# Kernel optimization log

Measured on AMD Instinct MI355X. Metric: run time of the kernel, lower is better.

Reference implementation:

```python
import jax, jax.numpy as jnp
import numpy as np

B, S, D = 2, 2048, 1024
H, L = 16, 64  # num_heads, latent_dim (head dim); head_dim = H*L = 1024
ROPE_BASE = 10000.0


def _rope_tables(seq_len, dim):
    inv_freq = 1.0 / (ROPE_BASE ** (2.0 * jnp.arange(0, dim // 2, dtype=jnp.float32) / dim))
    pos = jnp.arange(seq_len, dtype=jnp.float32)
    ang = pos[:, None] * inv_freq[None, :]           # [S, L/2]
    cos = jnp.cos(ang).reshape(1, seq_len, 1, dim // 2)
    sin = jnp.sin(ang).reshape(1, seq_len, 1, dim // 2)
    return cos, sin


def _apply_rope(t, cos, sin):
    # t: [B, S, H, L]; interleaved-pair rotation then concat halves (as in source)
    tr = t.reshape(*t.shape[:-1], -1, 2)             # [B,S,H,L/2,2]
    x0, x1 = tr[..., 0], tr[..., 1]
    out = jnp.concatenate([x0 * cos - x1 * sin, x0 * sin + x1 * cos], axis=-1)
    return out.reshape(t.shape)


def setup_inputs() -> dict:
    key = jax.random.key(0)
    ks = jax.random.split(key, 5)
    scale = 0.03  # ~xavier for 1024x1024
    return {
        "x": jax.random.normal(ks[0], (B, S, D), dtype=jnp.float32),
        "Wq": jax.random.normal(ks[1], (D, H * L), dtype=jnp.float32) * scale,
        "bq": jnp.zeros((H * L,), dtype=jnp.float32),
        "Wk": jax.random.normal(ks[2], (D, H * L), dtype=jnp.float32) * scale,
        "bk": jnp.zeros((H * L,), dtype=jnp.float32),
        "Wv": jax.random.normal(ks[3], (D, H * L), dtype=jnp.float32) * scale,
        "bv": jnp.zeros((H * L,), dtype=jnp.float32),
        "Wo": jax.random.normal(ks[4], (H * L, D), dtype=jnp.float32) * scale,
        "bo": jnp.zeros((D,), dtype=jnp.float32),
    }


def reference(x, Wq, bq, Wk, bk, Wv, bv, Wo, bo):
    b, s, _ = x.shape
    q = (x @ Wq + bq).reshape(b, s, H, L)
    k = (x @ Wk + bk).reshape(b, s, H, L)
    v = (x @ Wv + bv).reshape(b, s, H, L)
    cos, sin = _rope_tables(s, L)
    q = _apply_rope(q, cos, sin)
    k = _apply_rope(k, cos, sin)
    q = jnp.transpose(q, (0, 2, 1, 3))  # [B,H,S,L]
    k = jnp.transpose(k, (0, 2, 1, 3))
    v = jnp.transpose(v, (0, 2, 1, 3))
    scores = jnp.einsum('bnqd,bnkd->bnqk', q, k) / jnp.sqrt(jnp.float32(L))
    # causal mask: keep positions where key <= query
    causal = jnp.arange(s)[None, :] <= jnp.arange(s)[:, None]  # [S,S]
    scores = jnp.where(causal, scores, -1e9)
    attn = jax.nn.softmax(scores, axis=-1)
    attended = jnp.einsum('bnqk,bnkd->bnqd', attn, v)
    attended = jnp.transpose(attended, (0, 2, 1, 3)).reshape(b, s, H * L)
    return attended @ Wo + bo
```

## Files before the change

### kernel.cpp

```cpp
#include <hip/hip_runtime.h>
#include <hip/hip_bf16.h>

typedef __bf16 bf16_t;
typedef __bf16 bf16x2 __attribute__((ext_vector_type(2)));
typedef __bf16 bf16x4 __attribute__((ext_vector_type(4)));
typedef __bf16 bf16x8 __attribute__((ext_vector_type(8)));
typedef float  f32x4  __attribute__((ext_vector_type(4)));

#define GLDS16(gp, lp) __builtin_amdgcn_global_load_lds( \
    (const __attribute__((address_space(1))) void*)(gp), \
    (__attribute__((address_space(3))) void*)(lp), 16, 0, 0)

#define MFMA16(a, b, c) __builtin_amdgcn_mfma_f32_16x16x32_bf16((a), (b), (c), 0, 0, 0)

static constexpr int kB = 2, kS = 2048, kD = 1024, kH = 16, kL = 64;
static constexpr int kM = kB * kS;
static constexpr int kNqkv = 3 * kD;
static constexpr int kBH = kB * kH;

__global__ void cast_x_kernel(const float* __restrict__ x, bf16_t* __restrict__ xb) {
    int i = blockIdx.x * 256 + threadIdx.x;
    float4 v = ((const float4*)x)[i];
    bf16x4 o;
    o[0] = (bf16_t)v.x; o[1] = (bf16_t)v.y; o[2] = (bf16_t)v.z; o[3] = (bf16_t)v.w;
    ((bf16x4*)xb)[i] = o;
}

__global__ void wtrans_kernel(const float* __restrict__ Wq, const float* __restrict__ Wk,
                              const float* __restrict__ Wv, const float* __restrict__ Wo,
                              bf16_t* __restrict__ Wqkv, bf16_t* __restrict__ WoT) {
    __shared__ float t[32 * 33];
    const int z = blockIdx.z;
    const float* W = (z == 0) ? Wq : (z == 1) ? Wk : (z == 2) ? Wv : Wo;
    bf16_t* Wt = (z < 3) ? (Wqkv + (size_t)z * 1024 * 1024) : WoT;
    const int k0 = blockIdx.x * 32, n0 = blockIdx.y * 32;
    const int tid = threadIdx.x;
#pragma unroll
    for (int i = 0; i < 4; ++i) {
        int idx = i * 256 + tid;
        int r = idx >> 5, c = idx & 31;
        t[r * 33 + c] = W[(size_t)(k0 + r) * 1024 + n0 + c];
    }
    __syncthreads();
#pragma unroll
    for (int i = 0; i < 4; ++i) {
        int idx = i * 256 + tid;
        int r = idx >> 5, c = idx & 31;
        Wt[(size_t)(n0 + r) * 1024 + k0 + c] = (bf16_t)t[c * 33 + r];
    }
}

__global__ void rope_table_kernel(float* __restrict__ cosT, float* __restrict__ sinT) {
    int i = blockIdx.x * 256 + threadIdx.x;
    int s = i >> 5, j = i & 31;
    double inv = pow(10000.0, -2.0 * (double)j / 64.0);
    double ang = (double)s * inv;
    cosT[i] = (float)cos(ang);
    sinT[i] = (float)sin(ang);
}

template <int MODE>
__global__ __launch_bounds__(256, 2)
void gemm_bf16(const bf16_t* __restrict__ A, const bf16_t* __restrict__ Bt,
               void* __restrict__ Cout,
               const float* __restrict__ b0, const float* __restrict__ b1,
               const float* __restrict__ b2, int Ndim, int Kdim) {
    __shared__ __align__(16) bf16_t Alds[128 * 32];
    __shared__ __align__(16) bf16_t Blds[128 * 32];
    const int tid = threadIdx.x;
    const int lane = tid & 63;
    const int wid = tid >> 6;
    const int lo = lane & 15, hi = lane >> 4;
    const int bm = blockIdx.x, bn = blockIdx.y;
    const int wr = wid >> 1, wc = wid & 1;

    const int rowS = (wid * 2) * 16 + (lane >> 2);
    const int colE = (lane & 3) * 8;
    const bf16_t* gA0 = A + (size_t)(bm * 128 + rowS) * Kdim + colE;
    const bf16_t* gA1 = gA0 + (size_t)16 * Kdim;
    const bf16_t* gB0 = Bt + (size_t)(bn * 128 + rowS) * Kdim + colE;
    const bf16_t* gB1 = gB0 + (size_t)16 * Kdim;
    bf16_t* lA0 = &Alds[(wid * 2) * 512];
    bf16_t* lA1 = &Alds[(wid * 2 + 1) * 512];
    bf16_t* lB0 = &Blds[(wid * 2) * 512];
    bf16_t* lB1 = &Blds[(wid * 2 + 1) * 512];

    f32x4 acc[4][4];
#pragma unroll
    for (int m = 0; m < 4; ++m)
#pragma unroll
        for (int n = 0; n < 4; ++n) acc[m][n] = (f32x4){0.f, 0.f, 0.f, 0.f};

    const int nk = Kdim >> 5;
    for (int kt = 0; kt < nk; ++kt) {
        const int k0 = kt * 32;
        GLDS16(gA0 + k0, lA0);
        GLDS16(gA1 + k0, lA1);
        GLDS16(gB0 + k0, lB0);
        GLDS16(gB1 + k0, lB1);
        __syncthreads();
        bf16x8 aF[4], bF[4];
#pragma unroll
        for (int m = 0; m < 4; ++m)
            aF[m] = *(const bf16x8*)&Alds[(wr * 64 + m * 16 + lo) * 32 + hi * 8];
#pragma unroll
        for (int n = 0; n < 4; ++n)
            bF[n] = *(const bf16x8*)&Blds[(wc * 64 + n * 16 + lo) * 32 + hi * 8];
#pragma unroll
        for (int m = 0; m < 4; ++m)
#pragma unroll
            for (int n = 0; n < 4; ++n)
                acc[m][n] = MFMA16(aF[m], bF[n], acc[m][n]);
        __syncthreads();
    }

    const int rbase = bm * 128 + wr * 64 + hi * 4;
    const int cbase = bn * 128 + wc * 64 + lo;
    if (MODE == 0) {
        bf16_t* C = (bf16_t*)Cout;
#pragma unroll
        for (int m = 0; m < 4; ++m)
#pragma unroll
            for (int n = 0; n < 4; ++n) {
                const int col = cbase + n * 16;
                const float bias = (col < 1024) ? b0[col]
                                 : (col < 2048) ? b1[col - 1024] : b2[col - 2048];
#pragma unroll
                for (int r = 0; r < 4; ++r) {
                    const int row = rbase + m * 16 + r;
                    C[(size_t)row * Ndim + col] = (bf16_t)(acc[m][n][r] + bias);
                }
            }
    } else {
        float* C = (float*)Cout;
#pragma unroll
        for (int m = 0; m < 4; ++m)
#pragma unroll
            for (int n = 0; n < 4; ++n) {
                const int col = cbase + n * 16;
                const float bias = b0[col];
#pragma unroll
                for (int r = 0; r < 4; ++r) {
                    const int row = rbase + m * 16 + r;
                    C[(size_t)row * Ndim + col] = acc[m][n][r] + bias;
                }
            }
    }
}

__global__ __launch_bounds__(256)
void rope_qk_kernel(const bf16_t* __restrict__ qkv,
                    const float* __restrict__ cosT,
                    const float* __restrict__ sinT,
                    bf16_t* __restrict__ Qr, bf16_t* __restrict__ Kr) {
    const int st = blockIdx.x, bh = blockIdx.y;
    const int b = bh >> 4, h = bh & 15;
    const int tid = threadIdx.x;
    const int r = tid >> 2;
    const int part = tid & 3;
    const int s = st * 64 + r;
    const int bs = b * kS + s;
    const bf16_t* qp = qkv + (size_t)bs * kNqkv + h * 64 + part * 16;
    const bf16_t* kp = qp + 1024;
    const size_t outoff = ((size_t)(b * kH + h) * kS + s) * 64;
    bf16_t* qo = Qr + outoff;
    char*   kob = (char*)(Kr + outoff);
    const float* cr = cosT + s * 32 + part * 8;
    const float* sr = sinT + s * 32 + part * 8;
    const float kScale = 0.125f * 1.44269504f;

    bf16x8 q0 = *(const bf16x8*)qp;
    bf16x8 q1 = *(const bf16x8*)(qp + 8);
    bf16x8 k0 = *(const bf16x8*)kp;
    bf16x8 k1 = *(const bf16x8*)(kp + 8);
    bf16x8 qlo, qhi, klo, khi;
#pragma unroll
    for (int j = 0; j < 8; ++j) {
        const float cv = cr[j];
        const float sv = sr[j];
        float qa, qb2, ka, kb2;
        if (j < 4) {
            qa = (float)q0[2 * j];     qb2 = (float)q0[2 * j + 1];
            ka = (float)k0[2 * j];     kb2 = (float)k0[2 * j + 1];
        } else {
            qa = (float)q1[2 * j - 8]; qb2 = (float)q1[2 * j - 7];
            ka = (float)k1[2 * j - 8]; kb2 = (float)k1[2 * j - 7];
        }
        qlo[j] = (bf16_t)((qa * cv - qb2 * sv) * kScale);
        qhi[j] = (bf16_t)((qa * sv + qb2 * cv) * kScale);
        klo[j] = (bf16_t)(ka * cv - kb2 * sv);
        khi[j] = (bf16_t)(ka * sv + kb2 * cv);
    }
    *(bf16x8*)(qo + part * 8)      = qlo;
    *(bf16x8*)(qo + 32 + part * 8) = qhi;
    const int sw = s & 7;
    *(bf16x8*)(kob + (((part)     ^ sw) << 4)) = klo;
    *(bf16x8*)(kob + (((part + 4) ^ sw) << 4)) = khi;
}

__global__ void vtrans_kernel(const bf16_t* __restrict__ qkv, bf16_t* __restrict__ VT) {
    __shared__ __align__(16) bf16_t t[64 * 72];
    const int st = blockIdx.x, bh = blockIdx.y;
    const int b = bh >> 4, h = bh & 15;
    const int tid = threadIdx.x;
    const int r = tid >> 2, g = tid & 3;
    const bf16_t* src = qkv + ((size_t)(b * kS + st * 64 + r)) * kNqkv + 2048 + h * 64 + g * 16;
    bf16x8 v0 = *(const bf16x8*)src;
    bf16x8 v1 = *(const bf16x8*)(src + 8);
    *(bf16x8*)&t[r * 72 + g * 16] = v0;
    *(bf16x8*)&t[r * 72 + g * 16 + 8] = v1;
    __syncthreads();
    bf16x8 o0, o1;
#pragma unroll
    for (int j = 0; j < 8; ++j) {
        o0[j] = t[(g * 16 + j) * 72 + r];
        o1[j] = t[(g * 16 + 8 + j) * 72 + r];
    }
    char* dstb = (char*)(VT + ((size_t)bh * 64 + r) * kS) + st * 128;
    const int sw = r & 7;
    *(bf16x8*)(dstb + (((g * 2)     ^ sw) << 4)) = o0;
    *(bf16x8*)(dstb + (((g * 2 + 1) ^ sw) << 4)) = o1;
}

__global__ __launch_bounds__(256, 4)
void attn_kernel(const bf16_t* __restrict__ Qr, const bf16_t* __restrict__ Kr,
                 const bf16_t* __restrict__ VT, bf16_t* __restrict__ attended) {
    __shared__ __align__(16) bf16_t Klds[2][64 * 64];
    __shared__ __align__(16) bf16_t Vlds[2][64 * 64];
    __shared__ __align__(16) bf16_t Plds[4][16 * 64];
    const int bh = blockIdx.x;
    const int y = blockIdx.y;
    const int qt = (y < 8) ? (31 - y) : (y < 16) ? (y + 8)
                 : (y < 24) ? (31 - y) : (y - 24);
    const int tid = threadIdx.x;
    const int lane = tid & 63, wid = tid >> 6;
    const int lo = lane & 15, hi = lane >> 4;
    const int q0 = qt * 64 + wid * 16;

    const char* Kg = (const char*)(Kr + (size_t)bh * kS * 64);
    const char* Vg = (const char*)(VT + (size_t)bh * 64 * kS);
    const bf16_t* Q = Qr + (size_t)bh * kS * 64;

    const bf16x8 aQ0 = *(const bf16x8*)&Q[(size_t)(q0 + lo) * 64 + hi * 8];
    const bf16x8 aQ1 = *(const bf16x8*)&Q[(size_t)(q0 + lo) * 64 + 32 + hi * 8];

    char* Pb = (char*)&Plds[wid][0];
    const int psw = (lo & 7) << 4;

    f32x4 O[4];
#pragma unroll
    for (int dt = 0; dt < 4; ++dt) O[dt] = (f32x4){0.f, 0.f, 0.f, 0.f};
    float m_run = -1e30f, l_run = 0.f;

    auto stage = [&](int buf, int t) {
        char* Kl = (char*)&Klds[buf][0];
        char* Vl = (char*)&Vlds[buf][0];
        const size_t kb = (size_t)t * 128 * 64;
        const int vcol = t * 128;
#pragma unroll
        for (int j = 0; j < 2; ++j) {
            const int seg = wid * 2 + j;
            GLDS16(Kg + kb + seg * 1024 + lane * 16, Kl + seg * 1024);
            const int row = seg * 8 + (lane >> 3);
            GLDS16(Vg + (size_t)row * (kS * 2) + vcol + (lane & 7) * 16, Vl + seg * 1024);
        }
    };

    stage(0, 0);
    int cur = 0;
    const int ntiles = qt + 1;
    for (int t = 0; t < ntiles; ++t) {
        __syncthreads();
        if (t + 1 < ntiles) stage(cur ^ 1, t + 1);
        const char* Kb = (const char*)&Klds[cur][0];
        const char* Vb = (const char*)&Vlds[cur][0];
        const int kv0 = t * 64;
        const bool edge = (t == qt);

        f32x4 s[4];
#pragma unroll
        for (int ct = 0; ct < 4; ++ct) s[ct] = (f32x4){0.f, 0.f, 0.f, 0.f};
        __builtin_amdgcn_s_setprio(1);
#pragma unroll
        for (int ct = 0; ct < 4; ++ct) {
            const int rr = ct * 16 + lo;
            const bf16x8 bK0 = *(const bf16x8*)(Kb + rr * 128 + (((hi)     ^ (rr & 7)) << 4));
            const bf16x8 bK1 = *(const bf16x8*)(Kb + rr * 128 + (((hi + 4) ^ (rr & 7)) << 4));
            s[ct] = MFMA16(bK0, aQ0, s[ct]);
            s[ct] = MFMA16(bK1, aQ1, s[ct]);
        }
        __builtin_amdgcn_s_setprio(0);

        if (edge) {
            const int qg = q0 + lo;
#pragma unroll
            for (int ct = 0; ct < 4; ++ct)
#pragma unroll
                for (int r = 0; r < 4; ++r)
                    if (kv0 + ct * 16 + hi * 4 + r > qg) s[ct][r] = -1e30f;
        }
        float pmax = -1e30f;
#pragma unroll
        for (int ct = 0; ct < 4; ++ct)
#pragma unroll
            for (int r = 0; r < 4; ++r) pmax = fmaxf(pmax, s[ct][r]);
        pmax = fmaxf(pmax, __shfl_xor(pmax, 16, 64));
        pmax = fmaxf(pmax, __shfl_xor(pmax, 32, 64));
        if (!__all(pmax - m_run <= 8.0f)) {
            const float mn = fmaxf(m_run, pmax);
            const float alpha = exp2f(m_run - mn);
            m_run = mn;
            l_run *= alpha;
            float av[4];
#pragma unroll
            for (int r = 0; r < 4; ++r) av[r] = __shfl(alpha, hi * 4 + r, 64);
#pragma unroll
            for (int dt = 0; dt < 4; ++dt)
#pragma unroll
                for (int r = 0; r < 4; ++r) O[dt][r] *= av[r];
        }
        float psum = 0.f;
#pragma unroll
        for (int ct = 0; ct < 4; ++ct)
#pragma unroll
            for (int r = 0; r < 4; ++r) {
                const float e = exp2f(s[ct][r] - m_run);
                s[ct][r] = e;
                psum += e;
            }
        psum += __shfl_xor(psum, 16, 64);
        psum += __shfl_xor(psum, 32, 64);
        l_run += psum;
#pragma unroll
        for (int ct = 0; ct < 4; ++ct)
#pragma unroll
            for (int rp = 0; rp < 2; ++rp) {
                bf16x2 v;
                v[0] = (bf16_t)s[ct][2 * rp];
                v[1] = (bf16_t)s[ct][2 * rp + 1];
                *(bf16x2*)(Pb + ((lo * 128 + (ct * 16 + hi * 4 + 2 * rp) * 2) ^ psw)) = v;
            }
        const bf16x8 aP0 = *(const bf16x8*)(Pb + ((lo * 128 + hi * 16) ^ psw));
        const bf16x8 aP1 = *(const bf16x8*)(Pb + ((lo * 128 + 64 + hi * 16) ^ psw));

        __builtin_amdgcn_s_setprio(1);
#pragma unroll
        for (int dt = 0; dt < 4; ++dt) {
            const int rr = dt * 16 + lo;
            const bf16x8 bV0 = *(const bf16x8*)(Vb + rr * 128 + (((hi)     ^ (rr & 7)) << 4));
            const bf16x8 bV1 = *(const bf16x8*)(Vb + rr * 128 + (((hi + 4) ^ (rr & 7)) << 4));
            O[dt] = MFMA16(aP0, bV0, O[dt]);
            O[dt] = MFMA16(aP1, bV1, O[dt]);
        }
        __builtin_amdgcn_s_setprio(0);
        cur ^= 1;
    }

    const int b = bh >> 4, h = bh & 15;
    float li[4];
#pragma unroll
    for (int r = 0; r < 4; ++r) li[r] = 1.0f / __shfl(l_run, hi * 4 + r, 64);
#pragma unroll
    for (int dt = 0; dt < 4; ++dt)
#pragma unroll
        for (int r = 0; r < 4; ++r) {
            const int row = q0 + hi * 4 + r;
            attended[((size_t)(b * kS + row)) * kD + h * 64 + dt * 16 + lo] =
                (bf16_t)(O[dt][r] * li[r]);
        }
}

extern "C" void kernel_launch(void* const* d_in, const int* in_sizes, int n_in,
                              void* d_out, int out_size, void* d_ws, size_t ws_size,
                              hipStream_t stream) {
    const float* x  = (const float*)d_in[0];
    const float* Wq = (const float*)d_in[1];
    const float* bq = (const float*)d_in[2];
    const float* Wk = (const float*)d_in[3];
    const float* bk = (const float*)d_in[4];
    const float* Wv = (const float*)d_in[5];
    const float* bv = (const float*)d_in[6];
    const float* Wo = (const float*)d_in[7];
    const float* bo = (const float*)d_in[8];
    float* out = (float*)d_out;

    char* ws = (char*)d_ws;
    size_t off = 0;
    auto carve = [&](size_t bytes) -> char* {
        char* p = ws + off;
        off += (bytes + 255) & ~(size_t)255;
        return p;
    };
    bf16_t* xb    = (bf16_t*)carve((size_t)kM * kD * 2);
    bf16_t* WqkvT = (bf16_t*)carve((size_t)kNqkv * kD * 2);
    bf16_t* WoT   = (bf16_t*)carve((size_t)kD * kD * 2);
    float*  cosT  = (float*)carve((size_t)kS * 32 * 4);
    float*  sinT  = (float*)carve((size_t)kS * 32 * 4);
    bf16_t* qkv   = (bf16_t*)carve((size_t)kM * kNqkv * 2);
    bf16_t* Qr    = (bf16_t*)carve((size_t)kBH * kS * 64 * 2);
    bf16_t* Kr    = (bf16_t*)carve((size_t)kBH * kS * 64 * 2);
    bf16_t* VT    = (bf16_t*)carve((size_t)kBH * kS * 64 * 2);
    bf16_t* att   = (bf16_t*)carve((size_t)kM * kD * 2);

    cast_x_kernel<<<(kM * kD) / (256 * 4), 256, 0, stream>>>(x, xb);
    wtrans_kernel<<<dim3(32, 32, 4), 256, 0, stream>>>(Wq, Wk, Wv, Wo, WqkvT, WoT);
    rope_table_kernel<<<(kS * 32) / 256, 256, 0, stream>>>(cosT, sinT);

    gemm_bf16<0><<<dim3(kM / 128, kNqkv / 128), 256, 0, stream>>>(
        xb, WqkvT, qkv, bq, bk, bv, kNqkv, kD);

    rope_qk_kernel<<<dim3(kS / 64, kBH), 256, 0, stream>>>(qkv, cosT, sinT, Qr, Kr);
    vtrans_kernel<<<dim3(kS / 64, kBH), 256, 0, stream>>>(qkv, VT);

    attn_kernel<<<dim3(kBH, 32), 256, 0, stream>>>(Qr, Kr, VT, att);

    gemm_bf16<1><<<dim3(kM / 128, kD / 128), 256, 0, stream>>>(
        att, WoT, out, bo, nullptr, nullptr, kD, kD);
}
```

Measured before the change: 130.3 us.

## Switch attention to 32x32 MFMA with two 32-row query waves per block

The attention kernel moves from 16x16x32 MFMA tiles (4 waves, 16 query rows each) to 32x32x16 MFMA tiles with 2 waves of 32 query rows each. Block size drops to 128 threads, and each wave stages twice as many K/V segments. The softmax then runs on 16-register accumulators with one cross-half shuffle, the per-row alpha shuffles go away, and the output is stored as vectorized bf16x4. The aim is fewer LDS reads per FLOP and less softmax bookkeeping, at the cost of higher register pressure and fewer waves per block for latency hiding.

```diff
diff --git a/kernel.cpp b/kernel.cpp
--- a/kernel.cpp
+++ b/kernel.cpp
@@ -6,12 +6,14 @@
 typedef __bf16 bf16x4 __attribute__((ext_vector_type(4)));
 typedef __bf16 bf16x8 __attribute__((ext_vector_type(8)));
 typedef float  f32x4  __attribute__((ext_vector_type(4)));
+typedef float  f32x16 __attribute__((ext_vector_type(16)));
 
 #define GLDS16(gp, lp) __builtin_amdgcn_global_load_lds( \
     (const __attribute__((address_space(1))) void*)(gp), \
     (__attribute__((address_space(3))) void*)(lp), 16, 0, 0)
 
 #define MFMA16(a, b, c) __builtin_amdgcn_mfma_f32_16x16x32_bf16((a), (b), (c), 0, 0, 0)
+#define MFMA32(a, b, c) __builtin_amdgcn_mfma_f32_32x32x16_bf16((a), (b), (c), 0, 0, 0)
 
 static constexpr int kB = 2, kS = 2048, kD = 1024, kH = 16, kL = 64;
 static constexpr int kM = kB * kS;
@@ -222,34 +224,35 @@
     *(bf16x8*)(dstb + (((g * 2 + 1) ^ sw) << 4)) = o1;
 }
 
-__global__ __launch_bounds__(256, 4)
+__global__ __launch_bounds__(128, 2)
 void attn_kernel(const bf16_t* __restrict__ Qr, const bf16_t* __restrict__ Kr,
                  const bf16_t* __restrict__ VT, bf16_t* __restrict__ attended) {
     __shared__ __align__(16) bf16_t Klds[2][64 * 64];
     __shared__ __align__(16) bf16_t Vlds[2][64 * 64];
-    __shared__ __align__(16) bf16_t Plds[4][16 * 64];
+    __shared__ __align__(16) bf16_t Plds[2][32 * 64];
     const int bh = blockIdx.x;
     const int y = blockIdx.y;
     const int qt = (y < 8) ? (31 - y) : (y < 16) ? (y + 8)
                  : (y < 24) ? (31 - y) : (y - 24);
     const int tid = threadIdx.x;
     const int lane = tid & 63, wid = tid >> 6;
-    const int lo = lane & 15, hi = lane >> 4;
-    const int q0 = qt * 64 + wid * 16;
+    const int lo5 = lane & 31, hi2 = lane >> 5;
+    const int q0 = qt * 64 + wid * 32;
+    const int qg = q0 + lo5;
 
     const char* Kg = (const char*)(Kr + (size_t)bh * kS * 64);
     const char* Vg = (const char*)(VT + (size_t)bh * 64 * kS);
     const bf16_t* Q = Qr + (size_t)bh * kS * 64;
 
-    const bf16x8 aQ0 = *(const bf16x8*)&Q[(size_t)(q0 + lo) * 64 + hi * 8];
-    const bf16x8 aQ1 = *(const bf16x8*)&Q[(size_t)(q0 + lo) * 64 + 32 + hi * 8];
+    bf16x8 aQ[4];
+#pragma unroll
+    for (int ds = 0; ds < 4; ++ds)
+        aQ[ds] = *(const bf16x8*)&Q[(size_t)qg * 64 + ds * 16 + hi2 * 8];
 
     char* Pb = (char*)&Plds[wid][0];
-    const int psw = (lo & 7) << 4;
-
-    f32x4 O[4];
-#pragma unroll
-    for (int dt = 0; dt < 4; ++dt) O[dt] = (f32x4){0.f, 0.f, 0.f, 0.f};
+    const int psw = (lo5 & 7) << 4;
+
+    f32x16 O0 = 0.f, O1 = 0.f;
     float m_run = -1e30f, l_run = 0.f;
 
     auto stage = [&](int buf, int t) {
@@ -258,8 +261,8 @@
         const size_t kb = (size_t)t * 128 * 64;
         const int vcol = t * 128;
 #pragma unroll
-        for (int j = 0; j < 2; ++j) {
-            const int seg = wid * 2 + j;
+        for (int j = 0; j < 4; ++j) {
+            const int seg = wid * 4 + j;
             GLDS16(Kg + kb + seg * 1024 + lane * 16, Kl + seg * 1024);
             const int row = seg * 8 + (lane >> 3);
             GLDS16(Vg + (size_t)row * (kS * 2) + vcol + (lane & 7) * 16, Vl + seg * 1024);
@@ -277,97 +280,88 @@
         const int kv0 = t * 64;
         const bool edge = (t == qt);
 
-        f32x4 s[4];
-#pragma unroll
-        for (int ct = 0; ct < 4; ++ct) s[ct] = (f32x4){0.f, 0.f, 0.f, 0.f};
+#pragma unroll
+        for (int kvg = 0; kvg < 2; ++kvg) {
+            f32x16 s = 0.f;
+            const int krow = kvg * 32 + lo5;
+            const int ksw = (krow & 7);
+            __builtin_amdgcn_s_setprio(1);
+#pragma unroll
+            for (int ds = 0; ds < 4; ++ds) {
+                const bf16x8 aK = *(const bf16x8*)(Kb + krow * 128 + (((ds * 2 + hi2) ^ ksw) << 4));
+                s = MFMA32(aK, aQ[ds], s);
+            }
+            __builtin_amdgcn_s_setprio(0);
+
+            const int kvb = kv0 + kvg * 32 + 4 * hi2;
+            if (edge) {
+#pragma unroll
+                for (int reg = 0; reg < 16; ++reg)
+                    if (kvb + (reg & 3) + 8 * (reg >> 2) > qg) s[reg] = -1e30f;
+            }
+            float pmax = -1e30f;
+#pragma unroll
+            for (int reg = 0; reg < 16; ++reg) pmax = fmaxf(pmax, s[reg]);
+            pmax = fmaxf(pmax, __shfl_xor(pmax, 32, 64));
+            if (!__all(pmax - m_run <= 8.0f)) {
+                const float mn = fmaxf(m_run, pmax);
+                const float alpha = exp2f(m_run - mn);
+                m_run = mn;
+                l_run *= alpha;
+                O0 = O0 * alpha;
+                O1 = O1 * alpha;
+            }
+            float psum = 0.f;
+#pragma unroll
+            for (int reg = 0; reg < 16; ++reg) {
+                const float e = exp2f(s[reg] - m_run);
+                s[reg] = e;
+                psum += e;
+            }
+            psum += __shfl_xor(psum, 32, 64);
+            l_run += psum;
+#pragma unroll
+            for (int quad = 0; quad < 4; ++quad) {
+                bf16x4 v;
+#pragma unroll
+                for (int r = 0; r < 4; ++r) v[r] = (bf16_t)s[quad * 4 + r];
+                *(bf16x4*)(Pb + ((lo5 * 128 + kvg * 64 + quad * 16 + hi2 * 8) ^ psw)) = v;
+            }
+        }
+
+        bf16x8 pf[4];
+#pragma unroll
+        for (int ks = 0; ks < 4; ++ks)
+            pf[ks] = *(const bf16x8*)(Pb + ((lo5 * 128 + ks * 32 + hi2 * 16) ^ psw));
+
+        const int vsw0 = (lo5 & 7);
         __builtin_amdgcn_s_setprio(1);
 #pragma unroll
-        for (int ct = 0; ct < 4; ++ct) {
-            const int rr = ct * 16 + lo;
-            const bf16x8 bK0 = *(const bf16x8*)(Kb + rr * 128 + (((hi)     ^ (rr & 7)) << 4));
-            const bf16x8 bK1 = *(const bf16x8*)(Kb + rr * 128 + (((hi + 4) ^ (rr & 7)) << 4));
-            s[ct] = MFMA16(bK0, aQ0, s[ct]);
-            s[ct] = MFMA16(bK1, aQ1, s[ct]);
-        }
-        __builtin_amdgcn_s_setprio(0);
-
-        if (edge) {
-            const int qg = q0 + lo;
-#pragma unroll
-            for (int ct = 0; ct < 4; ++ct)
-#pragma unroll
-                for (int r = 0; r < 4; ++r)
-                    if (kv0 + ct * 16 + hi * 4 + r > qg) s[ct][r] = -1e30f;
-        }
-        float pmax = -1e30f;
-#pragma unroll
-        for (int ct = 0; ct < 4; ++ct)
-#pragma unroll
-            for (int r = 0; r < 4; ++r) pmax = fmaxf(pmax, s[ct][r]);
-        pmax = fmaxf(pmax, __shfl_xor(pmax, 16, 64));
-        pmax = fmaxf(pmax, __shfl_xor(pmax, 32, 64));
-        if (!__all(pmax - m_run <= 8.0f)) {
-            const float mn = fmaxf(m_run, pmax);
-            const float alpha = exp2f(m_run - mn);
-            m_run = mn;
-            l_run *= alpha;
-            float av[4];
-#pragma unroll
-            for (int r = 0; r < 4; ++r) av[r] = __shfl(alpha, hi * 4 + r, 64);
-#pragma unroll
-            for (int dt = 0; dt < 4; ++dt)
-#pragma unroll
-                for (int r = 0; r < 4; ++r) O[dt][r] *= av[r];
-        }
-        float psum = 0.f;
-#pragma unroll
-        for (int ct = 0; ct < 4; ++ct)
-#pragma unroll
-            for (int r = 0; r < 4; ++r) {
-                const float e = exp2f(s[ct][r] - m_run);
-                s[ct][r] = e;
-                psum += e;
-            }
-        psum += __shfl_xor(psum, 16, 64);
-        psum += __shfl_xor(psum, 32, 64);
-        l_run += psum;
-#pragma unroll
-        for (int ct = 0; ct < 4; ++ct)
-#pragma unroll
-            for (int rp = 0; rp < 2; ++rp) {
-                bf16x2 v;
-                v[0] = (bf16_t)s[ct][2 * rp];
-                v[1] = (bf16_t)s[ct][2 * rp + 1];
-                *(bf16x2*)(Pb + ((lo * 128 + (ct * 16 + hi * 4 + 2 * rp) * 2) ^ psw)) = v;
-            }
-        const bf16x8 aP0 = *(const bf16x8*)(Pb + ((lo * 128 + hi * 16) ^ psw));
-        const bf16x8 aP1 = *(const bf16x8*)(Pb + ((lo * 128 + 64 + hi * 16) ^ psw));
-
-        __builtin_amdgcn_s_setprio(1);
-#pragma unroll
-        for (int dt = 0; dt < 4; ++dt) {
-            const int rr = dt * 16 + lo;
-            const bf16x8 bV0 = *(const bf16x8*)(Vb + rr * 128 + (((hi)     ^ (rr & 7)) << 4));
-            const bf16x8 bV1 = *(const bf16x8*)(Vb + rr * 128 + (((hi + 4) ^ (rr & 7)) << 4));
-            O[dt] = MFMA16(aP0, bV0, O[dt]);
-            O[dt] = MFMA16(aP1, bV1, O[dt]);
+        for (int ks = 0; ks < 4; ++ks) {
+            const bf16x8 aV0 = *(const bf16x8*)(Vb + lo5 * 128 + (((ks * 2 + hi2) ^ vsw0) << 4));
+            O0 = MFMA32(aV0, pf[ks], O0);
+            const bf16x8 aV1 = *(const bf16x8*)(Vb + (32 + lo5) * 128 + (((ks * 2 + hi2) ^ vsw0) << 4));
+            O1 = MFMA32(aV1, pf[ks], O1);
         }
         __builtin_amdgcn_s_setprio(0);
         cur ^= 1;
     }
 
     const int b = bh >> 4, h = bh & 15;
-    float li[4];
-#pragma unroll
-    for (int r = 0; r < 4; ++r) li[r] = 1.0f / __shfl(l_run, hi * 4 + r, 64);
-#pragma unroll
-    for (int dt = 0; dt < 4; ++dt)
+    const float li = 1.0f / l_run;
+    bf16_t* outp = attended + ((size_t)(b * kS + qg)) * kD + h * 64;
+#pragma unroll
+    for (int quad = 0; quad < 4; ++quad) {
+        bf16x4 v0, v1;
 #pragma unroll
         for (int r = 0; r < 4; ++r) {
-            const int row = q0 + hi * 4 + r;
-            attended[((size_t)(b * kS + row)) * kD + h * 64 + dt * 16 + lo] =
-                (bf16_t)(O[dt][r] * li[r]);
+            v0[r] = (bf16_t)(O0[quad * 4 + r] * li);
+            v1[r] = (bf16_t)(O1[quad * 4 + r] * li);
         }
+        const int d0 = 8 * quad + 4 * hi2;
+        *(bf16x4*)(outp + d0) = v0;
+        *(bf16x4*)(outp + 32 + d0) = v1;
+    }
 }
 
 extern "C" void kernel_launch(void* const* d_in, const int* in_sizes, int n_in,
@@ -412,7 +406,7 @@
     rope_qk_kernel<<<dim3(kS / 64, kBH), 256, 0, stream>>>(qkv, cosT, sinT, Qr, Kr);
     vtrans_kernel<<<dim3(kS / 64, kBH), 256, 0, stream>>>(qkv, VT);
 
-    attn_kernel<<<dim3(kBH, 32), 256, 0, stream>>>(Qr, Kr, VT, att);
+    attn_kernel<<<dim3(kBH, 32), 128, 0, stream>>>(Qr, Kr, VT, att);
 
     gemm_bf16<1><<<dim3(kM / 128, kD / 128), 256, 0, stream>>>(
         att, WoT, out, bo, nullptr, nullptr, kD, kD);
```

Result: slower. 146.2 us (+12.2%).
